# Kernel tuning notes

Hardware: AMD Instinct MI355X
Metric: run time of the kernel (lower is better)

## Reference

```python
import jax, jax.numpy as jnp
import numpy as np

B, D_IN, D_OUT, N_CACHE = 2048, 1024, 512, 50000


def setup_inputs() -> dict:
    key = jax.random.key(0)
    k1, k2, k3, k4, k5 = jax.random.split(key, 5)
    scale = 1.0 / np.sqrt(D_IN)
    return {
        "x": jax.random.normal(k1, (B, D_IN), dtype=jnp.float32),
        "W": jax.random.normal(k2, (D_OUT, D_IN), dtype=jnp.float32) * scale,
        "b": jax.random.normal(k3, (D_OUT,), dtype=jnp.float32) * 0.01,
        "cache_image_features": jax.random.normal(k4, (N_CACHE, D_OUT), dtype=jnp.float32),
        "cache_text_features": jax.random.normal(k5, (N_CACHE, D_OUT), dtype=jnp.float32),
        "beta": jnp.ones((1,), dtype=jnp.float32),
        "alpha": jnp.ones((1,), dtype=jnp.float32),
    }


def reference(x, W, b, cache_image_features, cache_text_features, beta, alpha):
    # projected_x = x @ W.T + b  -> [B, D_OUT]
    projected_x = jnp.einsum('bi,oi->bo', x, W) + b
    # similarity over cached image features -> [B, N_CACHE]
    similarity = jnp.einsum('bo,no->bn', projected_x, cache_image_features)
    weights = jax.nn.softmax(beta * similarity, axis=-1)
    # retrieve from cached text features -> [B, D_OUT]
    retrieved = jnp.einsum('bn,no->bo', weights, cache_text_features)
    return projected_x + alpha * retrieved
```

## Files before the change

### kernel.cpp

```cpp
#include <hip/hip_runtime.h>
#include <hip/hip_bf16.h>
#include <math.h>

typedef _Float16 f16;
typedef __attribute__((ext_vector_type(8))) _Float16 f16x8;
typedef __attribute__((ext_vector_type(4))) float f32x4;
typedef __attribute__((ext_vector_type(16))) float f32x16;
typedef __attribute__((ext_vector_type(4))) unsigned int u32x4;
typedef __attribute__((ext_vector_type(2))) unsigned int u32x2;

#define MFMA16(A, B, C) __builtin_amdgcn_mfma_f32_16x16x32_f16(A, B, C, 0, 0, 0)
#define MFMA32(A, B, C) __builtin_amdgcn_mfma_f32_32x32x16_f16(A, B, C, 0, 0, 0)
#define AS1 __attribute__((address_space(1)))
#define AS3 __attribute__((address_space(3)))

__device__ __forceinline__ void gld16(const char* g, char* l) {
  __builtin_amdgcn_global_load_lds((const AS1 void*)g, (AS3 void*)l, 16, 0, 0);
}

__device__ __forceinline__ unsigned pk2(float a, float b) {
  f16 x = (f16)a, y = (f16)b;
  unsigned short ux = __builtin_bit_cast(unsigned short, x);
  unsigned short uy = __builtin_bit_cast(unsigned short, y);
  return (unsigned)ux | ((unsigned)uy << 16);
}

namespace {
constexpr int kB = 2048;
constexpr int kNch = 16, kChunk = 3125, kNit = 98;
constexpr int kKRows = 50176;
constexpr int kVStride = 3200;
constexpr size_t WS_PROJ = 0;
constexpr size_t WS_QHI  = WS_PROJ + (size_t)2048 * 512 * 4;
constexpr size_t WS_M    = WS_QHI + (size_t)2048 * 512 * 2;
constexpr size_t WS_L    = WS_M + (size_t)kNch * kB * 4;
constexpr size_t WS_PV   = WS_L + (size_t)kNch * kB * 4;
constexpr size_t WS_K16  = WS_PV + (size_t)kNch * kB * 512 * 2;
constexpr size_t WS_VT   = WS_K16 + (size_t)kKRows * 512 * 2;
constexpr int LDS_K0 = 0, LDS_K1 = 33280;
constexpr int LDS_V0 = 66560, LDS_V1 = 99328;
constexpr int LDS_SXP = 132096;
constexpr int LDS_FAC = 148480;
constexpr int LDS_FLG = 148992;
constexpr int LDS_SZ  = 149504;
}

__global__ __launch_bounds__(256) void convk_kernel(const float* __restrict__ src,
                                                    f16* __restrict__ dst) {
  const size_t e = ((size_t)blockIdx.x * 256 + threadIdx.x) * 8;
  const int row = (int)(e >> 9);
  float4 a = make_float4(0.f, 0.f, 0.f, 0.f), b = a;
  if (row < 50000) {
    a = *(const float4*)(src + e);
    b = *(const float4*)(src + e + 4);
  }
  f16x8 h;
  h[0] = (f16)a.x; h[1] = (f16)a.y; h[2] = (f16)a.z; h[3] = (f16)a.w;
  h[4] = (f16)b.x; h[5] = (f16)b.y; h[6] = (f16)b.z; h[7] = (f16)b.w;
  *(f16x8*)(dst + e) = h;
}

__global__ __launch_bounds__(256) void transv_kernel(const float* __restrict__ Vf,
                                                     f16* __restrict__ Vt) {
  __shared__ float tile[64][65];
  const int kt = blockIdx.x, colt = blockIdx.y, ch = blockIdx.z;
  const int t = threadIdx.x;
  const int kbase = kt * 64, col0 = colt * 64;
  {
    const int key = t >> 2, cseg = (t & 3) * 16;
    const int kk = kbase + key;
    float4 v0 = make_float4(0.f, 0.f, 0.f, 0.f), v1 = v0, v2 = v0, v3 = v0;
    if (kk < kChunk) {
      const float* s = Vf + (size_t)(ch * kChunk + kk) * 512 + col0 + cseg;
      v0 = *(const float4*)(s);
      v1 = *(const float4*)(s + 4);
      v2 = *(const float4*)(s + 8);
      v3 = *(const float4*)(s + 12);
    }
    float* tr = &tile[key][cseg];
    tr[0] = v0.x;  tr[1] = v0.y;  tr[2] = v0.z;  tr[3] = v0.w;
    tr[4] = v1.x;  tr[5] = v1.y;  tr[6] = v1.z;  tr[7] = v1.w;
    tr[8] = v2.x;  tr[9] = v2.y;  tr[10] = v2.z; tr[11] = v2.w;
    tr[12] = v3.x; tr[13] = v3.y; tr[14] = v3.z; tr[15] = v3.w;
  }
  __syncthreads();
  {
    const int col = t >> 2, kw = (t & 3) * 16;
    f16x8 h0, h1;
    #pragma unroll
    for (int u = 0; u < 8; u++) h0[u] = (f16)tile[kw + u][col];
    #pragma unroll
    for (int u = 0; u < 8; u++) h1[u] = (f16)tile[kw + 8 + u][col];
    f16* d = Vt + ((size_t)ch * 512 + col0 + col) * kVStride + kbase + kw;
    *(f16x8*)(d) = h0;
    *(f16x8*)(d + 8) = h1;
  }
}

__global__ __launch_bounds__(256) void gemm1_kernel(
    const float* __restrict__ x, const float* __restrict__ W,
    const float* __restrict__ bias, float* __restrict__ proj,
    f16* __restrict__ qhi)
{
  __shared__ f16 xh[2][64][40], xl[2][64][40], wh[2][64][40], wl[2][64][40];
  const int t = threadIdx.x;
  const int lane = t & 63, w = t >> 6;
  const int wr = w >> 1, wc = w & 1;
  const int g = lane >> 4, j = lane & 15;
  const int m0 = blockIdx.x * 64, n0 = blockIdx.y * 64;
  const int srow = t >> 2;
  const int soff = (t & 3) * 8;

  const f32x4 fzero = {0.f, 0.f, 0.f, 0.f};
  f32x4 acc[2][2], acc2[2][2];
  #pragma unroll
  for (int a = 0; a < 2; a++)
    #pragma unroll
    for (int bb = 0; bb < 2; bb++) { acc[a][bb] = fzero; acc2[a][bb] = fzero; }

  auto stage = [&](int k0s, int buf) {
    const float* xs  = x + (size_t)(m0 + srow) * 1024 + k0s + soff;
    const float* wsr = W + (size_t)(n0 + srow) * 1024 + k0s + soff;
    f16x8 hx, lx, hw, lw;
    #pragma unroll
    for (int i = 0; i < 8; i++) {
      float v = xs[i];
      f16 h = (f16)v;
      hx[i] = h;
      lx[i] = (f16)((v - (float)h) * 2048.0f);
      float u = wsr[i];
      f16 hu = (f16)u;
      hw[i] = hu;
      lw[i] = (f16)((u - (float)hu) * 2048.0f);
    }
    *(f16x8*)&xh[buf][srow][soff] = hx;
    *(f16x8*)&xl[buf][srow][soff] = lx;
    *(f16x8*)&wh[buf][srow][soff] = hw;
    *(f16x8*)&wl[buf][srow][soff] = lw;
  };

  stage(0, 0);
  for (int ks = 0; ks < 32; ks++) {
    __syncthreads();
    if (ks < 31) stage((ks + 1) * 32, (ks + 1) & 1);
    const int buf = ks & 1;
    f16x8 ah[2], al[2], bh[2], bl[2];
    #pragma unroll
    for (int mf = 0; mf < 2; mf++) {
      const int r = wr * 32 + mf * 16 + j;
      ah[mf] = *(const f16x8*)&xh[buf][r][g * 8];
      al[mf] = *(const f16x8*)&xl[buf][r][g * 8];
      const int cc = wc * 32 + mf * 16 + j;
      bh[mf] = *(const f16x8*)&wh[buf][cc][g * 8];
      bl[mf] = *(const f16x8*)&wl[buf][cc][g * 8];
    }
    #pragma unroll
    for (int mf = 0; mf < 2; mf++)
      #pragma unroll
      for (int nf = 0; nf < 2; nf++) {
        acc[mf][nf]  = MFMA16(ah[mf], bh[nf], acc[mf][nf]);
        acc2[mf][nf] = MFMA16(ah[mf], bl[nf], acc2[mf][nf]);
        acc2[mf][nf] = MFMA16(al[mf], bh[nf], acc2[mf][nf]);
      }
  }

  #pragma unroll
  for (int mf = 0; mf < 2; mf++)
    #pragma unroll
    for (int nf = 0; nf < 2; nf++)
      #pragma unroll
      for (int r = 0; r < 4; r++) {
        const int m = m0 + wr * 32 + mf * 16 + g * 4 + r;
        const int n = n0 + wc * 32 + nf * 16 + j;
        float p = acc[mf][nf][r] + acc2[mf][nf][r] * (1.0f / 2048.0f) + bias[n];
        proj[(size_t)m * 512 + n] = p;
        qhi[(size_t)m * 512 + n] = (f16)p;
      }
}

__global__ __launch_bounds__(512, 2) void attn_kernel(
    const f16* __restrict__ K16, const f16* __restrict__ Vt16,
    const f16* __restrict__ qhi_ws, const float* __restrict__ beta_p,
    float* __restrict__ m_part, float* __restrict__ l_part,
    f16* __restrict__ pvn)
{
  extern __shared__ char smem[];
  const int t = threadIdx.x, lane = t & 63, w = t >> 6;
  const int c = lane & 31, h = lane >> 5;
  const int qb = w & 3, dh = w >> 2;
  const int qp = w & 1, cq = w >> 1;
  const int ch = blockIdx.x & 15, qt = blockIdx.x >> 4;
  const int q0 = qt * 128;
  const float beta = beta_p[0];

  char* const Kb0 = smem + LDS_K0;
  char* const Kb1 = smem + LDS_K1;
  char* const Vb0 = smem + LDS_V0;
  char* const Vb1 = smem + LDS_V1;
  char* const SxPq = smem + LDS_SXP + qb * 4096;
  float* const facl = (float*)(smem + LDS_FAC);
  int* const flg = (int*)(smem + LDS_FLG);

  f16x8 Qf[16];
  {
    const f16* qsrc = qhi_ws + (size_t)(q0 + qb * 32 + c) * 512 + dh * 256 + h * 8;
    #pragma unroll
    for (int i = 0; i < 16; i++) Qf[i] = *(const f16x8*)(qsrc + i * 16);
  }
  __builtin_amdgcn_sched_barrier(0);

  const char* const Kg = (const char*)K16 + (size_t)(ch * kChunk) * 1024;
  const char* const Vg = (const char*)Vt16 + (size_t)ch * 512 * (kVStride * 2);
  const int vlo = (((lane & 3) ^ ((lane >> 3) & 3)) << 4);

  auto stageK = [&](int it, char* dstbuf) {
    const char* src = Kg + (size_t)(it * 32 + w * 4) * 1024 + lane * 16;
    char* dst = dstbuf + (w * 4) * 1040 + lane * 16;
    #pragma unroll
    for (int u = 0; u < 4; u++) gld16(src + u * 1024, dst + u * 1040);
  };
  auto stageV = [&](int it, char* dstbuf) {
    const char* src = Vg + (size_t)(w * 64 + (lane >> 2)) * (kVStride * 2) + it * 64 + vlo;
    char* dst = dstbuf + (w * 64) * 64 + lane * 16;
    #pragma unroll
    for (int u = 0; u < 4; u++)
      gld16(src + (size_t)(u * 16) * (kVStride * 2), dst + u * 1024);
  };

  const int kroff = c * 1040 + dh * 512 + h * 16;
  const int vbase = (cq * 128 + c) * 64;
  const int vswz = ((c >> 1) & 3) << 4;
  const int voff0 = (0 + h * 16) ^ vswz;
  const int voff1 = (32 + h * 16) ^ vswz;
  const char* const slotA = smem + LDS_SXP + (2 * qp) * 4096 + lane * 16;
  const char* const slotB = smem + LDS_SXP + (2 * qp + 1) * 4096 + lane * 16;

  f32x16 O[2][4];
  #pragma unroll
  for (int ql = 0; ql < 2; ql++)
    #pragma unroll
    for (int cb = 0; cb < 4; cb++)
      #pragma unroll
      for (int r = 0; r < 16; r++) O[ql][cb][r] = 0.f;
  float mrow = -INFINITY, lrow = 0.f;

  stageK(0, Kb0);
  stageV(0, Vb0);
  asm volatile("s_waitcnt vmcnt(0)" ::: "memory");
  __builtin_amdgcn_s_barrier();

  for (int it = 0; it < kNit; it++) {
    const int p = it & 1;
    const char* const Kp = (p ? Kb1 : Kb0) + kroff;
    const char* const Vp = (p ? Vb1 : Vb0) + vbase;
    if (it + 1 < kNit) {
      stageK(it + 1, p ? Kb0 : Kb1);
      stageV(it + 1, p ? Vb0 : Vb1);
    }

    f32x16 S;
    #pragma unroll
    for (int r = 0; r < 16; r++) S[r] = 0.f;
    __builtin_amdgcn_s_setprio(1);
    #pragma unroll
    for (int i = 0; i < 16; i++) {
      f16x8 a = *(const f16x8*)(Kp + i * 32);
      S = MFMA32(a, Qf[i], S);
    }
    __builtin_amdgcn_s_setprio(0);

    if (dh == 1) {
      f32x4 v0 = {S[0], S[1], S[2], S[3]};
      f32x4 v1 = {S[4], S[5], S[6], S[7]};
      f32x4 v2 = {S[8], S[9], S[10], S[11]};
      f32x4 v3 = {S[12], S[13], S[14], S[15]};
      *(f32x4*)(SxPq + 0 * 1024 + lane * 16) = v0;
      *(f32x4*)(SxPq + 1 * 1024 + lane * 16) = v1;
      *(f32x4*)(SxPq + 2 * 1024 + lane * 16) = v2;
      *(f32x4*)(SxPq + 3 * 1024 + lane * 16) = v3;
    }
    asm volatile("s_waitcnt lgkmcnt(0)" ::: "memory");
    __builtin_amdgcn_s_barrier();

    if (dh == 0) {
      #pragma unroll
      for (int cc = 0; cc < 4; cc++) {
        f32x4 v = *(const f32x4*)(SxPq + cc * 1024 + lane * 16);
        S[4 * cc + 0] += v.x; S[4 * cc + 1] += v.y;
        S[4 * cc + 2] += v.z; S[4 * cc + 3] += v.w;
      }
      #pragma unroll
      for (int r = 0; r < 16; r++) S[r] *= beta;
      if (it == kNit - 1) {
        #pragma unroll
        for (int r = 0; r < 16; r++) {
          const int key = it * 32 + (r & 3) + 8 * (r >> 2) + 4 * h;
          if (key >= kChunk) S[r] = -INFINITY;
        }
      }
      float pm = S[0];
      #pragma unroll
      for (int r = 1; r < 16; r++) pm = fmaxf(pm, S[r]);
      pm = fmaxf(pm, __shfl_xor(pm, 32));
      const int need = __any(pm > mrow + 8.0f);
      float fc = 1.0f;
      if (need) {
        const float mn = fmaxf(mrow, pm);
        fc = __expf(mrow - mn);
        mrow = mn;
      }
      float pr[16], rs = 0.f;
      #pragma unroll
      for (int r = 0; r < 16; r++) { pr[r] = __expf(S[r] - mrow); rs += pr[r]; }
      rs += __shfl_xor(rs, 32);
      lrow = lrow * fc + rs;
      unsigned pA0 = pk2(pr[0], pr[1]),  pA1 = pk2(pr[2], pr[3]);
      unsigned pB0 = pk2(pr[4], pr[5]),  pB1 = pk2(pr[6], pr[7]);
      unsigned pC0 = pk2(pr[8], pr[9]),  pC1 = pk2(pr[10], pr[11]);
      unsigned pD0 = pk2(pr[12], pr[13]), pD1 = pk2(pr[14], pr[15]);
      unsigned sA0 = __shfl_xor(pA0, 32), sA1 = __shfl_xor(pA1, 32);
      unsigned sB0 = __shfl_xor(pB0, 32), sB1 = __shfl_xor(pB1, 32);
      unsigned sC0 = __shfl_xor(pC0, 32), sC1 = __shfl_xor(pC1, 32);
      unsigned sD0 = __shfl_xor(pD0, 32), sD1 = __shfl_xor(pD1, 32);
      u32x4 B0, B1;
      B0[0] = h ? sB0 : pA0;  B0[1] = h ? sB1 : pA1;
      B0[2] = h ? pB0 : sA0;  B0[3] = h ? pB1 : sA1;
      B1[0] = h ? sD0 : pC0;  B1[1] = h ? sD1 : pC1;
      B1[2] = h ? pD0 : sC0;  B1[3] = h ? pD1 : sC1;
      *(u32x4*)(SxPq + 0 * 1024 + lane * 16) = B0;
      *(u32x4*)(SxPq + 1 * 1024 + lane * 16) = B1;
      if (need && h == 0) facl[qb * 32 + c] = fc;
      if (lane == 0) flg[qb] = need;
    }
    asm volatile("s_waitcnt lgkmcnt(0)" ::: "memory");
    __builtin_amdgcn_s_barrier();

    const int f0 = flg[2 * qp];
    const int f1 = flg[2 * qp + 1];
    const f16x8 pb00 = *(const f16x8*)(slotA);
    const f16x8 pb01 = *(const f16x8*)(slotA + 1024);
    const f16x8 pb10 = *(const f16x8*)(slotB);
    const f16x8 pb11 = *(const f16x8*)(slotB + 1024);
    if (f0) {
      const float fc0 = facl[(2 * qp) * 32 + c];
      #pragma unroll
      for (int cb = 0; cb < 4; cb++)
        #pragma unroll
        for (int r = 0; r < 16; r++) O[0][cb][r] *= fc0;
    }
    if (f1) {
      const float fc1 = facl[(2 * qp + 1) * 32 + c];
      #pragma unroll
      for (int cb = 0; cb < 4; cb++)
        #pragma unroll
        for (int r = 0; r < 16; r++) O[1][cb][r] *= fc1;
    }
    __builtin_amdgcn_s_setprio(1);
    #pragma unroll
    for (int cb = 0; cb < 4; cb++) {
      f16x8 a0 = *(const f16x8*)(Vp + cb * 2048 + voff0);
      f16x8 a1 = *(const f16x8*)(Vp + cb * 2048 + voff1);
      O[0][cb] = MFMA32(a0, pb00, O[0][cb]);
      O[0][cb] = MFMA32(a1, pb01, O[0][cb]);
      O[1][cb] = MFMA32(a0, pb10, O[1][cb]);
      O[1][cb] = MFMA32(a1, pb11, O[1][cb]);
    }
    __builtin_amdgcn_s_setprio(0);

    asm volatile("s_waitcnt vmcnt(0)" ::: "memory");
    __builtin_amdgcn_s_barrier();
  }

  if (dh == 0) {
    const float iv = 1.0f / lrow;
    if (lane < 32) {
      m_part[ch * kB + q0 + qb * 32 + c] = mrow;
      l_part[ch * kB + q0 + qb * 32 + c] = lrow;
      facl[qb * 32 + c] = iv;
    }
  }
  asm volatile("s_waitcnt lgkmcnt(0)" ::: "memory");
  __builtin_amdgcn_s_barrier();
  const float iv0 = facl[(2 * qp) * 32 + c];
  const float iv1 = facl[(2 * qp + 1) * 32 + c];

  const size_t pvb = ((size_t)ch * kB + q0) * 512;
  #pragma unroll
  for (int ql = 0; ql < 2; ql++) {
    const int qrow = (2 * qp + ql) * 32 + c;
    const float iv = ql ? iv1 : iv0;
    #pragma unroll
    for (int cb = 0; cb < 4; cb++) {
      const int C = cq * 128 + cb * 32;
      #pragma unroll
      for (int a = 0; a < 4; a++) {
        unsigned lo = pk2(O[ql][cb][4 * a + 0] * iv, O[ql][cb][4 * a + 1] * iv);
        unsigned hi = pk2(O[ql][cb][4 * a + 2] * iv, O[ql][cb][4 * a + 3] * iv);
        u32x2 v = {lo, hi};
        *(u32x2*)(pvn + pvb + (size_t)qrow * 512 + C + 8 * a + 4 * h) = v;
      }
    }
  }
}

__global__ __launch_bounds__(256) void combine_kernel(
    const float* __restrict__ proj, const float* __restrict__ m_part,
    const float* __restrict__ l_part, const f16* __restrict__ pvn,
    const float* __restrict__ alpha_p, float* __restrict__ out)
{
  const int row = blockIdx.x;
  const int t = threadIdx.x;
  const float alpha = alpha_p[0];
  float M = -INFINITY;
  #pragma unroll
  for (int c = 0; c < kNch; c++) M = fmaxf(M, m_part[c * kB + row]);
  float gl[kNch];
  float T = 0.f;
  #pragma unroll
  for (int c = 0; c < kNch; c++) {
    gl[c] = __expf(m_part[c * kB + row] - M) * l_part[c * kB + row];
    T += gl[c];
  }
  const float s = alpha / T;
  #pragma unroll
  for (int half = 0; half < 2; half++) {
    const int col = t + half * 256;
    float acc = 0.f;
    #pragma unroll
    for (int c = 0; c < kNch; c++)
      acc += gl[c] * (float)pvn[((size_t)c * kB + row) * 512 + col];
    out[(size_t)row * 512 + col] = proj[(size_t)row * 512 + col] + acc * s;
  }
}

extern "C" void kernel_launch(void* const* d_in, const int* in_sizes, int n_in,
                              void* d_out, int out_size, void* d_ws, size_t ws_size,
                              hipStream_t stream) {
  (void)in_sizes; (void)n_in; (void)out_size; (void)ws_size;
  const float* x     = (const float*)d_in[0];
  const float* W     = (const float*)d_in[1];
  const float* bias  = (const float*)d_in[2];
  const float* cimg  = (const float*)d_in[3];
  const float* ctxt  = (const float*)d_in[4];
  const float* beta  = (const float*)d_in[5];
  const float* alpha = (const float*)d_in[6];
  float* out = (float*)d_out;
  char* ws = (char*)d_ws;

  float* proj = (float*)(ws + WS_PROJ);
  f16*   qhi  = (f16*)(ws + WS_QHI);
  float* mp   = (float*)(ws + WS_M);
  float* lp   = (float*)(ws + WS_L);
  f16*   pvn  = (f16*)(ws + WS_PV);
  f16*   K16  = (f16*)(ws + WS_K16);
  f16*   Vt16 = (f16*)(ws + WS_VT);

  hipFuncSetAttribute((const void*)attn_kernel,
                      hipFuncAttributeMaxDynamicSharedMemorySize, LDS_SZ);

  convk_kernel<<<(kKRows * 512 / 8 + 255) / 256, 256, 0, stream>>>(cimg, K16);
  transv_kernel<<<dim3(kVStride / 64, 8, kNch), 256, 0, stream>>>(ctxt, Vt16);
  gemm1_kernel<<<dim3(32, 8), 256, 0, stream>>>(x, W, bias, proj, qhi);
  attn_kernel<<<256, 512, LDS_SZ, stream>>>(K16, Vt16, qhi, beta, mp, lp, pvn);
  combine_kernel<<<2048, 256, 0, stream>>>(proj, mp, lp, pvn, alpha, out);
}
```

Before: 388.3 us.

## Software-pipeline PV step of previous tile with QK of current tile

Restructures the flash-attention loop so the P·V MFMA step for iteration it-1 runs at the top of iteration it, overlapping with the QK computation and removing one barrier per iteration. S and P now live in separate LDS regions so P from the previous step survives while the new S partials are written. V staging is deferred until after the first barrier and waits use partial vmcnt counts, so K and V loads can stay in flight longer. The change adds LDS usage and relies on careful vmcnt accounting for correctness.

```diff
diff --git a/kernel.cpp b/kernel.cpp
--- a/kernel.cpp
+++ b/kernel.cpp
@@ -39,10 +39,11 @@
 constexpr size_t WS_VT   = WS_K16 + (size_t)kKRows * 512 * 2;
 constexpr int LDS_K0 = 0, LDS_K1 = 33280;
 constexpr int LDS_V0 = 66560, LDS_V1 = 99328;
-constexpr int LDS_SXP = 132096;
-constexpr int LDS_FAC = 148480;
-constexpr int LDS_FLG = 148992;
-constexpr int LDS_SZ  = 149504;
+constexpr int LDS_S  = 132096;
+constexpr int LDS_P  = 148480;
+constexpr int LDS_FAC = 156672;
+constexpr int LDS_FLG = 157184;
+constexpr int LDS_SZ  = 157696;
 }
 
 __global__ __launch_bounds__(256) void convk_kernel(const float* __restrict__ src,
@@ -197,7 +198,8 @@
   char* const Kb1 = smem + LDS_K1;
   char* const Vb0 = smem + LDS_V0;
   char* const Vb1 = smem + LDS_V1;
-  char* const SxPq = smem + LDS_SXP + qb * 4096;
+  char* const Sq  = smem + LDS_S + qb * 4096;
+  char* const Pq  = smem + LDS_P + qb * 2048;
   float* const facl = (float*)(smem + LDS_FAC);
   int* const flg = (int*)(smem + LDS_FLG);
 
@@ -213,15 +215,15 @@
   const char* const Vg = (const char*)Vt16 + (size_t)ch * 512 * (kVStride * 2);
   const int vlo = (((lane & 3) ^ ((lane >> 3) & 3)) << 4);
 
-  auto stageK = [&](int it, char* dstbuf) {
-    const char* src = Kg + (size_t)(it * 32 + w * 4) * 1024 + lane * 16;
+  auto stageK = [&](int it2, char* dstbuf) {
+    const char* src = Kg + (size_t)(it2 * 32 + w * 4) * 1024 + lane * 16;
     char* dst = dstbuf + (w * 4) * 1040 + lane * 16;
     #pragma unroll
     for (int u = 0; u < 4; u++) gld16(src + u * 1024, dst + u * 1040);
   };
-  auto stageV = [&](int it, char* dstbuf) {
-    const char* src = Vg + (size_t)(w * 64 + (lane >> 2)) * (kVStride * 2) + it * 64 + vlo;
-    char* dst = dstbuf + (w * 64) * 64 + lane * 16;
+  auto stageV = [&](int it2, char* dstbuf) {
+    const char* src = Vg + (size_t)(w * 64 + (lane >> 2)) * (kVStride * 2) + it2 * 64 + vlo;
+    char* dst = dstbuf + (w * 4) * 1024 + lane * 16;
     #pragma unroll
     for (int u = 0; u < 4; u++)
       gld16(src + (size_t)(u * 16) * (kVStride * 2), dst + u * 1024);
@@ -232,8 +234,8 @@
   const int vswz = ((c >> 1) & 3) << 4;
   const int voff0 = (0 + h * 16) ^ vswz;
   const int voff1 = (32 + h * 16) ^ vswz;
-  const char* const slotA = smem + LDS_SXP + (2 * qp) * 4096 + lane * 16;
-  const char* const slotB = smem + LDS_SXP + (2 * qp + 1) * 4096 + lane * 16;
+  const char* const slotA = smem + LDS_P + (2 * qp) * 2048 + lane * 16;
+  const char* const slotB = smem + LDS_P + (2 * qp + 1) * 2048 + lane * 16;
 
   f32x16 O[2][4];
   #pragma unroll
@@ -244,19 +246,51 @@
       for (int r = 0; r < 16; r++) O[ql][cb][r] = 0.f;
   float mrow = -INFINITY, lrow = 0.f;
 
+  auto pvstep = [&](const char* Vp) {
+    const int f0 = flg[2 * qp];
+    const int f1 = flg[2 * qp + 1];
+    const f16x8 pb00 = *(const f16x8*)(slotA);
+    const f16x8 pb01 = *(const f16x8*)(slotA + 1024);
+    const f16x8 pb10 = *(const f16x8*)(slotB);
+    const f16x8 pb11 = *(const f16x8*)(slotB + 1024);
+    if (f0) {
+      const float fc0 = facl[(2 * qp) * 32 + c];
+      #pragma unroll
+      for (int cb = 0; cb < 4; cb++)
+        #pragma unroll
+        for (int r = 0; r < 16; r++) O[0][cb][r] *= fc0;
+    }
+    if (f1) {
+      const float fc1 = facl[(2 * qp + 1) * 32 + c];
+      #pragma unroll
+      for (int cb = 0; cb < 4; cb++)
+        #pragma unroll
+        for (int r = 0; r < 16; r++) O[1][cb][r] *= fc1;
+    }
+    __builtin_amdgcn_s_setprio(1);
+    #pragma unroll
+    for (int cb = 0; cb < 4; cb++) {
+      f16x8 a0 = *(const f16x8*)(Vp + cb * 2048 + voff0);
+      f16x8 a1 = *(const f16x8*)(Vp + cb * 2048 + voff1);
+      O[0][cb] = MFMA32(a0, pb00, O[0][cb]);
+      O[0][cb] = MFMA32(a1, pb01, O[0][cb]);
+      O[1][cb] = MFMA32(a0, pb10, O[1][cb]);
+      O[1][cb] = MFMA32(a1, pb11, O[1][cb]);
+    }
+    __builtin_amdgcn_s_setprio(0);
+  };
+
   stageK(0, Kb0);
   stageV(0, Vb0);
-  asm volatile("s_waitcnt vmcnt(0)" ::: "memory");
+  asm volatile("s_waitcnt vmcnt(4)" ::: "memory");
   __builtin_amdgcn_s_barrier();
 
   for (int it = 0; it < kNit; it++) {
     const int p = it & 1;
     const char* const Kp = (p ? Kb1 : Kb0) + kroff;
-    const char* const Vp = (p ? Vb1 : Vb0) + vbase;
-    if (it + 1 < kNit) {
-      stageK(it + 1, p ? Kb0 : Kb1);
-      stageV(it + 1, p ? Vb0 : Vb1);
-    }
+
+    if (it > 0) pvstep((p ? Vb0 : Vb1) + vbase);
+    if (it + 1 < kNit) stageK(it + 1, p ? Kb0 : Kb1);
 
     f32x16 S;
     #pragma unroll
@@ -274,18 +308,20 @@
       f32x4 v1 = {S[4], S[5], S[6], S[7]};
       f32x4 v2 = {S[8], S[9], S[10], S[11]};
       f32x4 v3 = {S[12], S[13], S[14], S[15]};
-      *(f32x4*)(SxPq + 0 * 1024 + lane * 16) = v0;
-      *(f32x4*)(SxPq + 1 * 1024 + lane * 16) = v1;
-      *(f32x4*)(SxPq + 2 * 1024 + lane * 16) = v2;
-      *(f32x4*)(SxPq + 3 * 1024 + lane * 16) = v3;
+      *(f32x4*)(Sq + 0 * 1024 + lane * 16) = v0;
+      *(f32x4*)(Sq + 1 * 1024 + lane * 16) = v1;
+      *(f32x4*)(Sq + 2 * 1024 + lane * 16) = v2;
+      *(f32x4*)(Sq + 3 * 1024 + lane * 16) = v3;
     }
     asm volatile("s_waitcnt lgkmcnt(0)" ::: "memory");
     __builtin_amdgcn_s_barrier();
 
+    if (it + 1 < kNit) stageV(it + 1, p ? Vb0 : Vb1);
+
     if (dh == 0) {
       #pragma unroll
       for (int cc = 0; cc < 4; cc++) {
-        f32x4 v = *(const f32x4*)(SxPq + cc * 1024 + lane * 16);
+        f32x4 v = *(const f32x4*)(Sq + cc * 1024 + lane * 16);
         S[4 * cc + 0] += v.x; S[4 * cc + 1] += v.y;
         S[4 * cc + 2] += v.z; S[4 * cc + 3] += v.w;
       }
@@ -327,49 +363,19 @@
       B0[2] = h ? pB0 : sA0;  B0[3] = h ? pB1 : sA1;
       B1[0] = h ? sD0 : pC0;  B1[1] = h ? sD1 : pC1;
       B1[2] = h ? pD0 : sC0;  B1[3] = h ? pD1 : sC1;
-      *(u32x4*)(SxPq + 0 * 1024 + lane * 16) = B0;
-      *(u32x4*)(SxPq + 1 * 1024 + lane * 16) = B1;
+      *(u32x4*)(Pq + lane * 16) = B0;
+      *(u32x4*)(Pq + 1024 + lane * 16) = B1;
       if (need && h == 0) facl[qb * 32 + c] = fc;
       if (lane == 0) flg[qb] = need;
     }
-    asm volatile("s_waitcnt lgkmcnt(0)" ::: "memory");
+    if (it + 1 < kNit)
+      asm volatile("s_waitcnt lgkmcnt(0) vmcnt(4)" ::: "memory");
+    else
+      asm volatile("s_waitcnt lgkmcnt(0) vmcnt(0)" ::: "memory");
     __builtin_amdgcn_s_barrier();
-
-    const int f0 = flg[2 * qp];
-    const int f1 = flg[2 * qp + 1];
-    const f16x8 pb00 = *(const f16x8*)(slotA);
-    const f16x8 pb01 = *(const f16x8*)(slotA + 1024);
-    const f16x8 pb10 = *(const f16x8*)(slotB);
-    const f16x8 pb11 = *(const f16x8*)(slotB + 1024);
-    if (f0) {
-      const float fc0 = facl[(2 * qp) * 32 + c];
-      #pragma unroll
-      for (int cb = 0; cb < 4; cb++)
-        #pragma unroll
-        for (int r = 0; r < 16; r++) O[0][cb][r] *= fc0;
-    }
-    if (f1) {
-      const float fc1 = facl[(2 * qp + 1) * 32 + c];
-      #pragma unroll
-      for (int cb = 0; cb < 4; cb++)
-        #pragma unroll
-        for (int r = 0; r < 16; r++) O[1][cb][r] *= fc1;
-    }
-    __builtin_amdgcn_s_setprio(1);
-    #pragma unroll
-    for (int cb = 0; cb < 4; cb++) {
-      f16x8 a0 = *(const f16x8*)(Vp + cb * 2048 + voff0);
-      f16x8 a1 = *(const f16x8*)(Vp + cb * 2048 + voff1);
-      O[0][cb] = MFMA32(a0, pb00, O[0][cb]);
-      O[0][cb] = MFMA32(a1, pb01, O[0][cb]);
-      O[1][cb] = MFMA32(a0, pb10, O[1][cb]);
-      O[1][cb] = MFMA32(a1, pb11, O[1][cb]);
-    }
-    __builtin_amdgcn_s_setprio(0);
-
-    asm volatile("s_waitcnt vmcnt(0)" ::: "memory");
-    __builtin_amdgcn_s_barrier();
-  }
+  }
+
+  pvstep((((kNit - 1) & 1) ? Vb1 : Vb0) + vbase);
 
   if (dh == 0) {
     const float iv = 1.0f / lrow;
```

Result: faster. 371.2 us (-4.4%).
